# Kernel optimization log

Hardware: AMD Instinct MI355X
Metric: run time of the kernel (lower is better)

The kernel has to match this reference:

```python
import jax, jax.numpy as jnp
import numpy as np
import math

B, S, HID = 4, 512, 768
H, D = 12, 64          # heads, head_size
I = 3072               # intermediate_size
EPS = 1e-12


def setup_inputs() -> dict:
    key = jax.random.key(0)
    ks = jax.random.split(key, 16)
    std = 0.02
    inp = {
        'hidden_states': jax.random.normal(ks[0], (B, S, HID), jnp.float32),
        'attention_mask': jnp.zeros((B, 1, 1, S), jnp.float32),
        'Wq': jax.random.normal(ks[1], (HID, HID), jnp.float32) * std,
        'bq': jnp.zeros((HID,), jnp.float32),
        'Wk': jax.random.normal(ks[2], (HID, HID), jnp.float32) * std,
        'bk': jnp.zeros((HID,), jnp.float32),
        'Wv': jax.random.normal(ks[3], (HID, HID), jnp.float32) * std,
        'bv': jnp.zeros((HID,), jnp.float32),
        'Wo': jax.random.normal(ks[4], (H, D, HID), jnp.float32) * std,  # per-head w_o
        'bo': jnp.zeros((H, HID), jnp.float32),
        'w_kp': jax.nn.softmax(jax.random.normal(ks[5], (H,), jnp.float32)),
        'w_a': jax.nn.softmax(jax.random.normal(ks[6], (H,), jnp.float32)),
        'Wi': jax.random.normal(ks[7], (HID, I), jnp.float32) * std,
        'bi': jnp.zeros((I,), jnp.float32),
        'Wout': jax.random.normal(ks[8], (I, HID), jnp.float32) * std,
        'bout': jnp.zeros((HID,), jnp.float32),
        'gamma': jnp.ones((HID,), jnp.float32),
        'beta': jnp.zeros((HID,), jnp.float32),
    }
    return inp


def _layernorm(x, gamma, beta):
    u = x.mean(-1, keepdims=True)
    s = jnp.mean((x - u) ** 2, axis=-1, keepdims=True)
    return gamma * (x - u) / jnp.sqrt(s + EPS) + beta


def _gelu(x):
    return x * 0.5 * (1.0 + jax.lax.erf(x / math.sqrt(2.0)))


def reference(hidden_states, attention_mask, Wq, bq, Wk, bk, Wv, bv,
              Wo, bo, w_kp, w_a, Wi, bi, Wout, bout, gamma, beta):
    # self-attention (eval mode: no dropout, no head_mask)
    q = (hidden_states @ Wq + bq).reshape(B, S, H, D)
    k = (hidden_states @ Wk + bk).reshape(B, S, H, D)
    v = (hidden_states @ Wv + bv).reshape(B, S, H, D)
    scores = jnp.einsum('bqhd,bkhd->bhqk', q, k) / math.sqrt(D)
    scores = scores + attention_mask  # additive mask, broadcast [B,1,1,S]
    probs = jax.nn.softmax(scores, axis=-1)
    ctx = jnp.einsum('bhqk,bkhd->bqhd', probs, v)  # [B,S,H,D]

    # per-head output projection w_o[i]: 64 -> 768, scaled by kappa
    head_out = jnp.einsum('bqhd,hdm->bqhm', ctx, Wo) + bo  # [B,S,H,HID]
    x = w_kp[None, None, :, None] * head_out
    # shared intermediate (gelu) + output linear, applied per head stream
    inter = _gelu(jnp.einsum('bqhm,mi->bqhi', x, Wi) + bi)  # [B,S,H,I]
    out = jnp.einsum('bqhi,im->bqhm', inter, Wout) + bout   # [B,S,H,HID]
    out = (w_a[None, None, :, None] * out).sum(axis=2)      # sum over heads

    return _layernorm(hidden_states + out, gamma, beta)
```

## Files before the change

### kernel.cpp

```cpp
#include <hip/hip_runtime.h>
#include <hip/hip_bf16.h>
#include <math.h>

typedef __hip_bfloat16 bf16;
typedef __attribute__((ext_vector_type(4))) float f32x4;
typedef __attribute__((ext_vector_type(8))) short short8;
typedef __attribute__((ext_vector_type(4))) unsigned short u16x4;

#define HIDN 768
#define NTOK 2048
#define NH 12
#define HD 64
#define ISZ 3072
#define SEQ 512

__device__ __forceinline__ bf16 f2bf(float x){ return __float2bfloat16(x); }
__device__ __forceinline__ float bf2f(unsigned short u){ return __uint_as_float(((unsigned)u)<<16); }
__device__ __forceinline__ float gelu_fast(float x){
    float u = x*x;
    float g = fmaf(u, fmaf(u, 0.00340656f, -0.0530184f), 0.393242f);
    float phi = __builtin_amdgcn_fmed3f(fmaf(x, g, 0.5f), 0.f, 1.f);
    return x * phi;
}

__device__ __forceinline__ void gload16(const bf16* g, bf16* l){
    __builtin_amdgcn_global_load_lds(
        (const __attribute__((address_space(1))) unsigned int*)g,
        (__attribute__((address_space(3))) unsigned int*)l,
        16, 0, 0);
}

#define FENCE asm volatile("" ::: "memory")

template<int EPI>
__global__ __launch_bounds__(512)
void gemm_pipe(const bf16* __restrict__ A, const bf16* __restrict__ B,
               void* __restrict__ Cbase, const float* __restrict__ bias,
               int lda, int ldb, int ldc,
               long sAz, long sBz, long sCz)
{
    __shared__ __align__(16) char hlds[2*24576];
    int z = blockIdx.z;
    A += (long)z*sAz; B += (long)z*sBz;

    int nwg  = gridDim.x * gridDim.y;
    int orig = blockIdx.y * gridDim.x + blockIdx.x;
    int q8 = nwg >> 3, r8 = nwg & 7;
    int xcd = orig & 7, idx = orig >> 3;
    int wg = (xcd < r8 ? xcd*(q8+1) : r8*(q8+1) + (xcd-r8)*q8) + idx;
    int bn = wg % gridDim.x, bm = wg / gridDim.x;

    int t = threadIdx.x;
    int wave = t >> 6, lane = t & 63;
    int wm = (wave >> 1) << 5;
    int wn = (wave & 1) << 5;
    int lr = lane & 15, lg = lane >> 4;
    int x7 = lr & 7;
    int gb0 = ((lg    ) ^ x7) << 4;
    int gb1 = ((4 | lg) ^ x7) << 4;

    int srow = t >> 3;
    int glog = (t & 7) ^ (srow & 7);
    const bf16* Ag0 = A + (long)(bm*128 + srow)*lda + glog*8;
    const bf16* Ag1 = Ag0 + (long)64*lda;
    const bf16* Bg0 = B + (long)(bn*64 + srow)*ldb + glog*8;

#define PSTAGE(buf,kt) { \
    gload16(Ag0 + (kt)*64, (bf16*)(hlds + (buf)*24576 + t*16)); \
    gload16(Ag1 + (kt)*64, (bf16*)(hlds + (buf)*24576 + 8192 + t*16)); \
    gload16(Bg0 + (kt)*64, (bf16*)(hlds + (buf)*24576 + 16384 + t*16)); }

    PSTAGE(0, 0);

    f32x4 acc[2][2] = {};

    #pragma unroll
    for (int kt = 0; kt < 12; ++kt){
        if (kt < 11) PSTAGE((kt+1)&1, kt+1);
        if (kt < 11) asm volatile("s_waitcnt vmcnt(3)" ::: "memory");
        else         asm volatile("s_waitcnt vmcnt(0)" ::: "memory");
        FENCE; __builtin_amdgcn_s_barrier(); FENCE;

        const char* Lb = hlds + (kt&1)*24576;
        short8 af[2][2], bfr[2][2];
        #pragma unroll
        for (int m=0;m<2;m++){
            const char* pr = Lb + (wm + m*16 + lr)*128;
            af[m][0] = *(const short8*)(pr + gb0);
            af[m][1] = *(const short8*)(pr + gb1);
        }
        #pragma unroll
        for (int n=0;n<2;n++){
            const char* pr = Lb + 16384 + (wn + n*16 + lr)*128;
            bfr[n][0] = *(const short8*)(pr + gb0);
            bfr[n][1] = *(const short8*)(pr + gb1);
        }
        __builtin_amdgcn_s_setprio(1);
        #pragma unroll
        for (int m=0;m<2;m++)
            #pragma unroll
            for (int n=0;n<2;n++)
                #pragma unroll
                for (int kk=0;kk<2;kk++)
                    acc[m][n] = __builtin_amdgcn_mfma_f32_16x16x32_bf16(af[m][kk], bfr[n][kk], acc[m][n], 0,0,0);
        __builtin_amdgcn_s_setprio(0);
        FENCE; __builtin_amdgcn_s_barrier(); FENCE;
    }
#undef PSTAGE

    #pragma unroll
    for (int m=0;m<2;m++){
        #pragma unroll
        for (int n=0;n<2;n++){
            int col = bn*64 + wn + n*16 + lr;
            #pragma unroll
            for (int i=0;i<4;i++){
                long row = (long)bm*128 + wm + m*16 + lg*4 + i;
                ((bf16*)Cbase + (long)z*sCz)[row*ldc+col] = f2bf(acc[m][n][i]);
            }
        }
    }
}

__global__ __launch_bounds__(512)
void gemm_pre(const bf16* __restrict__ WiT, const bf16* __restrict__ Wobf,
              const bf16* __restrict__ bo_pad, const bf16* __restrict__ hbf,
              const bf16* __restrict__ WqkvT,
              bf16* __restrict__ WcT, float* __restrict__ bhc,
              bf16* __restrict__ qkv,
              const float* __restrict__ w_kp, const float* __restrict__ bi,
              const float* __restrict__ bqkv)
{
    __shared__ __align__(16) char hlds[2*24576];
    int bid = blockIdx.x;
    int mode, local, gx, nwg, ldc;
    const bf16 *A, *B;
    if (bid < 48){        mode=0; local=bid;     gx=48; nwg=48;  A=bo_pad; B=WiT;   ldc=ISZ; }
    else if (bid < 336){  mode=1; local=bid-48;  gx=12; nwg=288; A=WiT;    B=Wobf;  ldc=HIDN; }
    else {                mode=2; local=bid-336; gx=36; nwg=576; A=hbf;    B=WqkvT; ldc=3*HIDN; }

    int cpx = nwg >> 3;
    int wg = (local & 7)*cpx + (local >> 3);
    int bn = wg % gx, bm = wg / gx;

    int t = threadIdx.x;
    int wave = t >> 6, lane = t & 63;
    int wm = (wave >> 1) << 5;
    int wn = (wave & 1) << 5;
    int lr = lane & 15, lg = lane >> 4;
    int x7 = lr & 7;
    int gb0 = ((lg    ) ^ x7) << 4;
    int gb1 = ((4 | lg) ^ x7) << 4;

    int srow = t >> 3;
    int glog = (t & 7) ^ (srow & 7);
    const bf16* Ag0 = A + (long)(bm*128 + srow)*HIDN + glog*8;
    const bf16* Ag1 = Ag0 + (long)64*HIDN;
    const bf16* Bg0 = B + (long)(bn*64 + srow)*HIDN + glog*8;

#define PSTAGE(buf,kt) { \
    gload16(Ag0 + (kt)*64, (bf16*)(hlds + (buf)*24576 + t*16)); \
    gload16(Ag1 + (kt)*64, (bf16*)(hlds + (buf)*24576 + 8192 + t*16)); \
    gload16(Bg0 + (kt)*64, (bf16*)(hlds + (buf)*24576 + 16384 + t*16)); }

    PSTAGE(0, 0);

    f32x4 acc[2][2] = {};

    #pragma unroll
    for (int kt = 0; kt < 12; ++kt){
        if (kt < 11) PSTAGE((kt+1)&1, kt+1);
        if (kt < 11) asm volatile("s_waitcnt vmcnt(3)" ::: "memory");
        else         asm volatile("s_waitcnt vmcnt(0)" ::: "memory");
        FENCE; __builtin_amdgcn_s_barrier(); FENCE;

        const char* Lb = hlds + (kt&1)*24576;
        short8 af[2][2], bfr[2][2];
        #pragma unroll
        for (int m=0;m<2;m++){
            const char* pr = Lb + (wm + m*16 + lr)*128;
            af[m][0] = *(const short8*)(pr + gb0);
            af[m][1] = *(const short8*)(pr + gb1);
        }
        #pragma unroll
        for (int n=0;n<2;n++){
            const char* pr = Lb + 16384 + (wn + n*16 + lr)*128;
            bfr[n][0] = *(const short8*)(pr + gb0);
            bfr[n][1] = *(const short8*)(pr + gb1);
        }
        __builtin_amdgcn_s_setprio(1);
        #pragma unroll
        for (int m=0;m<2;m++)
            #pragma unroll
            for (int n=0;n<2;n++)
                #pragma unroll
                for (int kk=0;kk<2;kk++)
                    acc[m][n] = __builtin_amdgcn_mfma_f32_16x16x32_bf16(af[m][kk], bfr[n][kk], acc[m][n], 0,0,0);
        __builtin_amdgcn_s_setprio(0);
        FENCE; __builtin_amdgcn_s_barrier(); FENCE;
    }
#undef PSTAGE

    #pragma unroll
    for (int m=0;m<2;m++){
        #pragma unroll
        for (int n=0;n<2;n++){
            int col = bn*64 + wn + n*16 + lr;
            #pragma unroll
            for (int i=0;i<4;i++){
                long row = (long)bm*128 + wm + m*16 + lg*4 + i;
                float v = acc[m][n][i];
                if (mode == 0){
                    if (row < NH) bhc[row*ISZ+col] = fmaf(w_kp[row], v, bi[col]);
                } else if (mode == 1){
                    WcT[row*HIDN+col] = f2bf(v * w_kp[col>>6]);
                } else {
                    qkv[row*(3*HIDN)+col] = f2bf(v + bqkv[col]);
                }
            }
        }
    }
}

__global__ __launch_bounds__(256)
void flash_attn(const bf16* __restrict__ qkv, const bf16* __restrict__ Vt,
                const float* __restrict__ mask, bf16* __restrict__ ctx2)
{
    __shared__ __align__(16) char p_lds[4*2048];
    __shared__ float mrg[2][64][21];
    int z = blockIdx.y;
    int b = z / NH, h = z - b*NH;
    int t = threadIdx.x;
    int wave = t >> 6, lane = t & 63;
    int qg = wave >> 1, kh = wave & 1;
    int q0 = blockIdx.x*32 + qg*16;
    int lr = lane & 15, lg = lane >> 4;
    int x7 = lr & 7;
    int gb0 = ((lg    ) ^ x7) << 4;
    int gb1 = ((4 | lg) ^ x7) << 4;

    const bf16* Qp = qkv + (long)(b*SEQ + q0 + lr)*(3*HIDN) + h*HD + lg*8;
    short8 aq0 = *(const short8*)(Qp);
    short8 aq1 = *(const short8*)(Qp + 32);

    const bf16* Kb = qkv + (long)b*SEQ*(3*HIDN) + HIDN + h*HD + lg*8;
    const bf16* Vb = Vt + (long)z*HD*SEQ;
    const float* mb = mask + b*SEQ;
    char* pw = p_lds + wave*2048;

    f32x4 o[4] = {};
    float lsum[4] = {0.f,0.f,0.f,0.f};

    for (int kt = kh*4; kt < kh*4 + 4; ++kt){
        int kbase = kt*64;
        short8 bk0[4], bk1[4];
        #pragma unroll
        for (int nf=0;nf<4;nf++){
            const bf16* kp = Kb + (long)(kbase + nf*16 + lr)*(3*HIDN);
            bk0[nf] = *(const short8*)(kp);
            bk1[nf] = *(const short8*)(kp + 32);
        }
        f32x4 s[4] = {};
        #pragma unroll
        for (int nf=0;nf<4;nf++){
            s[nf] = __builtin_amdgcn_mfma_f32_16x16x32_bf16(aq0, bk0[nf], s[nf], 0,0,0);
            s[nf] = __builtin_amdgcn_mfma_f32_16x16x32_bf16(aq1, bk1[nf], s[nf], 0,0,0);
        }
        short8 bv0[4], bv1[4];
        #pragma unroll
        for (int nf=0;nf<4;nf++){
            const bf16* vp = Vb + (long)(nf*16 + lr)*SEQ + kbase + lg*8;
            bv0[nf] = *(const short8*)(vp);
            bv1[nf] = *(const short8*)(vp + 32);
        }
        #pragma unroll
        for (int nf=0;nf<4;nf++){
            float mk = mb[kbase + nf*16 + lr];
            int gk = nf*2 + (lr>>3);
            #pragma unroll
            for (int i=0;i<4;i++){
                int q = lg*4 + i;
                float e = __expf(fmaf(s[nf][i], 0.125f, mk));
                lsum[i] += e;
                *(bf16*)(pw + q*128 + ((gk ^ (q&7))<<4) + (lr&7)*2) = f2bf(e);
            }
        }
        short8 ap0 = *(const short8*)(pw + lr*128 + gb0);
        short8 ap1 = *(const short8*)(pw + lr*128 + gb1);
        #pragma unroll
        for (int nf=0;nf<4;nf++){
            o[nf] = __builtin_amdgcn_mfma_f32_16x16x32_bf16(ap0, bv0[nf], o[nf], 0,0,0);
            o[nf] = __builtin_amdgcn_mfma_f32_16x16x32_bf16(ap1, bv1[nf], o[nf], 0,0,0);
        }
    }

    if (kh == 1){
        float* m = &mrg[qg][lane][0];
        #pragma unroll
        for (int nf=0;nf<4;nf++)
            #pragma unroll
            for (int i=0;i<4;i++) m[nf*4+i] = o[nf][i];
        #pragma unroll
        for (int i=0;i<4;i++) m[16+i] = lsum[i];
    }
    __syncthreads();
    if (kh == 1) return;

    {
        const float* m = &mrg[qg][lane][0];
        #pragma unroll
        for (int nf=0;nf<4;nf++)
            #pragma unroll
            for (int i=0;i<4;i++) o[nf][i] += m[nf*4+i];
        #pragma unroll
        for (int i=0;i<4;i++) lsum[i] += m[16+i];
    }

    #pragma unroll
    for (int i=0;i<4;i++){
        float v = lsum[i];
        v += __shfl_xor(v, 1, 64);
        v += __shfl_xor(v, 2, 64);
        v += __shfl_xor(v, 4, 64);
        v += __shfl_xor(v, 8, 64);
        lsum[i] = __builtin_amdgcn_rcpf(v);
    }
    bf16* Cp = ctx2 + (long)(b*SEQ + q0)*HIDN + h*HD;
    #pragma unroll
    for (int nf=0;nf<4;nf++)
        #pragma unroll
        for (int i=0;i<4;i++)
            Cp[(long)(lg*4+i)*HIDN + nf*16 + lr] = f2bf(o[nf][i] * lsum[i]);
}

__global__ __launch_bounds__(512)
void gemm_heads(const bf16* __restrict__ A, const bf16* __restrict__ B,
                bf16* __restrict__ S, const float* __restrict__ bhc,
                const float* __restrict__ w_a)
{
    __shared__ __align__(16) char hlds[2*24576 + 3072];
    char* bhcl = hlds + 49152;

    int nwg  = gridDim.x * gridDim.y;
    int orig = blockIdx.y * gridDim.x + blockIdx.x;
    int cpx = nwg >> 3;
    int wg = (orig & 7)*cpx + (orig >> 3);
    int bn = wg % gridDim.x, bm = wg / gridDim.x;

    int t = threadIdx.x;
    int wave = t >> 6, lane = t & 63;
    int wm = (wave >> 1) << 5;
    int wn = (wave & 1) << 5;
    int lr = lane & 15, lg = lane >> 4;
    int x7 = lr & 7;
    int gb0 = ((lg    ) ^ x7) << 4;
    int gb1 = ((4 | lg) ^ x7) << 4;

    int srow = t >> 3;
    int glog = (t & 7) ^ (srow & 7);
    const bf16* Ag0 = A + (long)(bm*128 + srow)*HIDN + glog*8;
    const bf16* Ag1 = Ag0 + (long)64*HIDN;
    const bf16* Bg0 = B + (long)(bn*64 + srow)*HIDN + glog*8;

    float wav[NH];
    #pragma unroll
    for (int h=0;h<NH;h++) wav[h] = w_a[h];

    if (t < 192){
        const float* src = bhc + (t>>4)*ISZ + bn*64 + (t&15)*4;
        gload16((const bf16*)src, (bf16*)(bhcl + t*16));
    }

#define HSTAGE(buf,h) { \
    gload16(Ag0 + (h)*64, (bf16*)(hlds + (buf)*24576 + t*16)); \
    gload16(Ag1 + (h)*64, (bf16*)(hlds + (buf)*24576 + 8192 + t*16)); \
    gload16(Bg0 + (h)*64, (bf16*)(hlds + (buf)*24576 + 16384 + t*16)); }

    HSTAGE(0, 0);

    f32x4 acc[2][2] = {};
    f32x4 sacc[2][2] = {};

    #pragma unroll
    for (int h = 0; h < NH; ++h){
        if (h < NH-1) HSTAGE((h+1)&1, h+1);
        if (h > 0){
            float bh0 = *(const float*)(bhcl + (h-1)*256 + (wn+lr)*4);
            float bh1 = *(const float*)(bhcl + (h-1)*256 + (wn+16+lr)*4);
            #pragma unroll
            for (int m=0;m<2;m++)
                #pragma unroll
                for (int n=0;n<2;n++)
                    #pragma unroll
                    for (int i=0;i<4;i++){
                        float v = acc[m][n][i] + (n ? bh1 : bh0);
                        sacc[m][n][i] = fmaf(wav[h-1], gelu_fast(v), sacc[m][n][i]);
                        acc[m][n][i] = 0.f;
                    }
        }
        if (h < NH-1) asm volatile("s_waitcnt vmcnt(3)" ::: "memory");
        else          asm volatile("s_waitcnt vmcnt(0)" ::: "memory");
        FENCE; __builtin_amdgcn_s_barrier(); FENCE;

        const char* Lb = hlds + (h&1)*24576;
        short8 af[2][2], bfr[2][2];
        #pragma unroll
        for (int m=0;m<2;m++){
            const char* pr = Lb + (wm + m*16 + lr)*128;
            af[m][0] = *(const short8*)(pr + gb0);
            af[m][1] = *(const short8*)(pr + gb1);
        }
        #pragma unroll
        for (int n=0;n<2;n++){
            const char* pr = Lb + 16384 + (wn + n*16 + lr)*128;
            bfr[n][0] = *(const short8*)(pr + gb0);
            bfr[n][1] = *(const short8*)(pr + gb1);
        }
        __builtin_amdgcn_s_setprio(1);
        #pragma unroll
        for (int m=0;m<2;m++)
            #pragma unroll
            for (int n=0;n<2;n++)
                #pragma unroll
                for (int kk=0;kk<2;kk++)
                    acc[m][n] = __builtin_amdgcn_mfma_f32_16x16x32_bf16(af[m][kk], bfr[n][kk], acc[m][n], 0,0,0);
        __builtin_amdgcn_s_setprio(0);
        FENCE; __builtin_amdgcn_s_barrier(); FENCE;
    }
#undef HSTAGE

    {
        float bh0 = *(const float*)(bhcl + (NH-1)*256 + (wn+lr)*4);
        float bh1 = *(const float*)(bhcl + (NH-1)*256 + (wn+16+lr)*4);
        #pragma unroll
        for (int m=0;m<2;m++)
            #pragma unroll
            for (int n=0;n<2;n++)
                #pragma unroll
                for (int i=0;i<4;i++){
                    float v = acc[m][n][i] + (n ? bh1 : bh0);
                    sacc[m][n][i] = fmaf(wav[NH-1], gelu_fast(v), sacc[m][n][i]);
                }
    }

    #pragma unroll
    for (int m=0;m<2;m++)
        #pragma unroll
        for (int n=0;n<2;n++)
            #pragma unroll
            for (int i=0;i<4;i++){
                long row = (long)bm*128 + wm + m*16 + lg*4 + i;
                S[row*ISZ + bn*64 + wn + n*16 + lr] = f2bf(sacc[m][n][i]);
            }
}

#define NPREP (NTOK*HIDN + HIDN*HIDN + 128*HIDN + 3*HIDN)
__global__ __launch_bounds__(256)
void prep_all(const float* __restrict__ Wq, const float* __restrict__ Wk,
              const float* __restrict__ Wv, const float* __restrict__ Wi,
              const float* __restrict__ Wout,
              bf16* __restrict__ WqkvT, bf16* __restrict__ WiT,
              bf16* __restrict__ WoutT,
              const float* __restrict__ hidden, const float* __restrict__ Wo,
              const float* __restrict__ bq, const float* __restrict__ bk,
              const float* __restrict__ bv, const float* __restrict__ bo,
              bf16* __restrict__ hbf, bf16* __restrict__ Wobf,
              float* __restrict__ bqkv, bf16* __restrict__ bo_pad)
{
    __shared__ float tile[32][33];
    int bid = blockIdx.x;
    if (bid >= 6336){
        int i = (bid-6336)*256 + threadIdx.x;
        const int n1 = NTOK*HIDN, n2 = HIDN*HIDN, n3 = 128*HIDN;
        if (i < n1) hbf[i] = f2bf(hidden[i]);
        int j = i - n1;
        if (j >= 0 && j < n2) Wobf[j] = f2bf(Wo[j]);
        int k = i - n1 - n2;
        if (k >= 0 && k < n3) bo_pad[k] = (k < NH*HIDN) ? f2bf(bo[k]) : f2bf(0.f);
        int l = i - n1 - n2 - n3;
        if (l >= 0 && l < 3*HIDN)
            bqkv[l] = (l < HIDN) ? bq[l] : (l < 2*HIDN ? bk[l-HIDN] : bv[l-2*HIDN]);
        return;
    }
    const float* src; bf16* dst; int R, C, ct, rem;
    if (bid < 1728){
        int z = bid / 576; rem = bid - z*576;
        src = (z==0) ? Wq : ((z==1) ? Wk : Wv);
        dst = WqkvT + (long)z*HIDN*HIDN;
        R = HIDN; C = HIDN; ct = 24;
    } else if (bid < 4032){
        rem = bid - 1728; src = Wi; dst = WiT; R = HIDN; C = ISZ; ct = 96;
    } else {
        rem = bid - 4032; src = Wout; dst = WoutT; R = ISZ; C = HIDN; ct = 24;
    }
    int c0 = (rem % ct)*32, r0 = (rem / ct)*32;
    int tx = threadIdx.x & 31, ty = threadIdx.x >> 5;
    #pragma unroll
    for (int i=0;i<32;i+=8) tile[ty+i][tx] = src[(long)(r0+ty+i)*C + c0+tx];
    __syncthreads();
    #pragma unroll
    for (int i=0;i<32;i+=8) dst[(long)(c0+ty+i)*R + r0+tx] = f2bf(tile[tx][ty+i]);
}

__global__ __launch_bounds__(256)
void transpose_v(const bf16* __restrict__ qkv, bf16* __restrict__ Vt)
{
    __shared__ bf16 tile[32][33];
    int za = blockIdx.z; int b = za/NH, h = za - b*NH;
    const bf16* src = qkv + (long)b*SEQ*3*HIDN + 2*HIDN + h*HD;
    bf16* dst = Vt + (long)za*HD*SEQ;
    int d0 = blockIdx.x*32, s0 = blockIdx.y*32;
    int tx = threadIdx.x & 31, ty = threadIdx.x >> 5;
    #pragma unroll
    for (int i=0;i<32;i+=8) tile[ty+i][tx] = src[(long)(s0+ty+i)*(3*HIDN) + d0+tx];
    __syncthreads();
    #pragma unroll
    for (int i=0;i<32;i+=8) dst[(long)(d0+ty+i)*SEQ + s0+tx] = tile[tx][ty+i];
}

__global__ __launch_bounds__(192)
void add_ln(const float4* __restrict__ hidden, const u16x4* __restrict__ part,
            const float4* __restrict__ bout, const float* __restrict__ w_a,
            const float4* __restrict__ gamma, const float4* __restrict__ beta,
            float4* __restrict__ out)
{
    __shared__ float red[6];
    int row = blockIdx.x;
    int t = threadIdx.x;
    int wave = t >> 6, lane = t & 63;
    float swa = 0.f;
    #pragma unroll
    for (int h=0;h<NH;h++) swa += w_a[h];

    long idx = (long)row*192 + t;
    float4 x = hidden[idx];
    #pragma unroll
    for (int z=0;z<4;z++){
        u16x4 p = part[(long)z*NTOK*192 + idx];
        x.x += bf2f(p.x); x.y += bf2f(p.y); x.z += bf2f(p.z); x.w += bf2f(p.w);
    }
    float4 bo4 = bout[t];
    x.x += swa*bo4.x; x.y += swa*bo4.y; x.z += swa*bo4.z; x.w += swa*bo4.w;

    float sum = x.x + x.y + x.z + x.w;
    #pragma unroll
    for (int o=32;o>0;o>>=1) sum += __shfl_xor(sum,o,64);
    if (lane==0) red[wave] = sum;
    __syncthreads();
    sum = red[0] + red[1] + red[2];
    float u = sum * (1.0f/768.0f);

    float dx = x.x-u, dy = x.y-u, dz = x.z-u, dw = x.w-u;
    float vs = dx*dx + dy*dy + dz*dz + dw*dw;
    #pragma unroll
    for (int o=32;o>0;o>>=1) vs += __shfl_xor(vs,o,64);
    if (lane==0) red[3+wave] = vs;
    __syncthreads();
    vs = red[3] + red[4] + red[5];
    float rstd = rsqrtf(vs*(1.0f/768.0f) + 1e-12f);

    float4 g = gamma[t], b = beta[t];
    float4 r;
    r.x = g.x*dx*rstd + b.x;
    r.y = g.y*dy*rstd + b.y;
    r.z = g.z*dz*rstd + b.z;
    r.w = g.w*dw*rstd + b.w;
    out[idx] = r;
}

extern "C" void kernel_launch(void* const* d_in, const int* in_sizes, int n_in,
                              void* d_out, int out_size, void* d_ws, size_t ws_size,
                              hipStream_t stream)
{
    const float* hidden = (const float*)d_in[0];
    const float* mask   = (const float*)d_in[1];
    const float* Wq = (const float*)d_in[2];
    const float* bq = (const float*)d_in[3];
    const float* Wk = (const float*)d_in[4];
    const float* bk = (const float*)d_in[5];
    const float* Wv = (const float*)d_in[6];
    const float* bv = (const float*)d_in[7];
    const float* Wo = (const float*)d_in[8];
    const float* bo = (const float*)d_in[9];
    const float* w_kp = (const float*)d_in[10];
    const float* w_a  = (const float*)d_in[11];
    const float* Wi = (const float*)d_in[12];
    const float* bi = (const float*)d_in[13];
    const float* Wout = (const float*)d_in[14];
    const float* boutp = (const float*)d_in[15];
    const float* gamma = (const float*)d_in[16];
    const float* beta  = (const float*)d_in[17];
    float* out = (float*)d_out;

    char* w = (char*)d_ws;
    auto alloc = [&](size_t bytes)->char* {
        char* p = w; w += (bytes + 255) & ~(size_t)255; return p;
    };
    bf16*  hbf    = (bf16*) alloc((size_t)NTOK*HIDN*2);
    bf16*  WqkvT  = (bf16*) alloc((size_t)3*HIDN*HIDN*2);
    float* bqkv   = (float*)alloc((size_t)3*HIDN*4);
    bf16*  WiT    = (bf16*) alloc((size_t)ISZ*HIDN*2);
    bf16*  WoutT  = (bf16*) alloc((size_t)HIDN*ISZ*2);
    bf16*  Wobf   = (bf16*) alloc((size_t)HIDN*HIDN*2);
    bf16*  WcT    = (bf16*) alloc((size_t)ISZ*HIDN*2);
    bf16*  bo_pad = (bf16*) alloc((size_t)128*HIDN*2);
    float* bhc    = (float*)alloc((size_t)NH*ISZ*4);
    bf16*  part   = (bf16*) alloc((size_t)4*NTOK*HIDN*2);
    bf16*  qkv    = (bf16*) alloc((size_t)NTOK*3*HIDN*2);
    bf16*  ctx2   = (bf16*) alloc((size_t)NTOK*HIDN*2);
    bf16*  Sbuf   = (bf16*) alloc((size_t)NTOK*ISZ*2);
    bf16*  Vt     = (bf16*) alloc((size_t)NH*4*HD*SEQ*2);

    prep_all<<<6336 + (NPREP+255)/256, 256, 0, stream>>>(
        Wq, Wk, Wv, Wi, Wout, WqkvT, WiT, WoutT,
        hidden, Wo, bq, bk, bv, bo, hbf, Wobf, bqkv, bo_pad);

    gemm_pre<<<912, 512, 0, stream>>>(
        WiT, Wobf, bo_pad, hbf, WqkvT,
        WcT, bhc, qkv, w_kp, bi, bqkv);

    transpose_v<<<dim3(2,16,48), 256, 0, stream>>>(qkv, Vt);
    flash_attn<<<dim3(SEQ/32, 48), 256, 0, stream>>>(qkv, Vt, mask, ctx2);

    gemm_heads<<<dim3(ISZ/64, NTOK/128), 512, 0, stream>>>(
        ctx2, WcT, Sbuf, bhc, w_a);

    gemm_pipe<1><<<dim3(HIDN/64, NTOK/128, 4), 512, 0, stream>>>(
        Sbuf, WoutT, part, nullptr,
        ISZ, ISZ, HIDN,
        768, 768, (long)NTOK*HIDN);

    add_ln<<<NTOK, 192, 0, stream>>>(
        (const float4*)hidden, (const u16x4*)part, (const float4*)boutp,
        w_a, (const float4*)gamma, (const float4*)beta, (float4*)out);
}
```

Baseline: 110.5 us.

## Widen gemm_heads N tile from 64 to 96 columns per workgroup

Each workgroup of the per-head GEMM+GELU kernel now covers 96 output columns instead of 64, and each wave computes a 2x3 MFMA fragment grid instead of 2x2. This lets each A tile loaded from ctx2 be reused across more columns, cuts the grid from 768 to 512 workgroups, and lowers the A traffic per output. The bias table is now loaded synchronously into LDS, w_a is read per head instead of held in registers, and only six waves issue B loads, so the vmcnt waits become wave-dependent. The costs are more LDS and more accumulator registers per workgroup, with a possible loss of occupancy, and 512 workgroups may fill the CUs less evenly.

```diff
diff --git a/kernel.cpp b/kernel.cpp
--- a/kernel.cpp
+++ b/kernel.cpp
@@ -333,13 +333,13 @@
             Cp[(long)(lg*4+i)*HIDN + nf*16 + lr] = f2bf(o[nf][i] * lsum[i]);
 }
 
-__global__ __launch_bounds__(512)
+__global__ __launch_bounds__(512, 4)
 void gemm_heads(const bf16* __restrict__ A, const bf16* __restrict__ B,
                 bf16* __restrict__ S, const float* __restrict__ bhc,
                 const float* __restrict__ w_a)
 {
-    __shared__ __align__(16) char hlds[2*24576 + 3072];
-    char* bhcl = hlds + 49152;
+    __shared__ __align__(16) char hlds[2*28672 + 4608];
+    char* bhcl = hlds + 57344;
 
     int nwg  = gridDim.x * gridDim.y;
     int orig = blockIdx.y * gridDim.x + blockIdx.x;
@@ -350,7 +350,7 @@
     int t = threadIdx.x;
     int wave = t >> 6, lane = t & 63;
     int wm = (wave >> 1) << 5;
-    int wn = (wave & 1) << 5;
+    int wn = (wave & 1) * 48;
     int lr = lane & 15, lg = lane >> 4;
     int x7 = lr & 7;
     int gb0 = ((lg    ) ^ x7) << 4;
@@ -360,50 +360,59 @@
     int glog = (t & 7) ^ (srow & 7);
     const bf16* Ag0 = A + (long)(bm*128 + srow)*HIDN + glog*8;
     const bf16* Ag1 = Ag0 + (long)64*HIDN;
-    const bf16* Bg0 = B + (long)(bn*64 + srow)*HIDN + glog*8;
-
-    float wav[NH];
-    #pragma unroll
-    for (int h=0;h<NH;h++) wav[h] = w_a[h];
-
-    if (t < 192){
-        const float* src = bhc + (t>>4)*ISZ + bn*64 + (t&15)*4;
-        gload16((const bf16*)src, (bf16*)(bhcl + t*16));
-    }
+    const bf16* Bg0 = B + (long)(bn*96 + srow)*HIDN + glog*8;
+    const bf16* Bg1 = Bg0 + (long)48*HIDN;
+
+    if (t < 288){
+        int hh = t / 24, cc = (t % 24) * 4;
+        float4 v = *(const float4*)&bhc[hh*ISZ + bn*96 + cc];
+        *(float4*)(bhcl + t*16) = v;
+    }
+    asm volatile("s_waitcnt vmcnt(0)" ::: "memory");
 
 #define HSTAGE(buf,h) { \
-    gload16(Ag0 + (h)*64, (bf16*)(hlds + (buf)*24576 + t*16)); \
-    gload16(Ag1 + (h)*64, (bf16*)(hlds + (buf)*24576 + 8192 + t*16)); \
-    gload16(Bg0 + (h)*64, (bf16*)(hlds + (buf)*24576 + 16384 + t*16)); }
+    gload16(Ag0 + (h)*64, (bf16*)(hlds + (buf)*28672 + t*16)); \
+    gload16(Ag1 + (h)*64, (bf16*)(hlds + (buf)*28672 + 8192 + t*16)); \
+    if (wave < 6){ \
+        gload16(Bg0 + (h)*64, (bf16*)(hlds + (buf)*28672 + 16384 + t*16)); \
+        gload16(Bg1 + (h)*64, (bf16*)(hlds + (buf)*28672 + 22528 + t*16)); \
+    } }
 
     HSTAGE(0, 0);
 
-    f32x4 acc[2][2] = {};
-    f32x4 sacc[2][2] = {};
+    f32x4 acc[2][3] = {};
+    f32x4 sacc[2][3] = {};
 
     #pragma unroll
     for (int h = 0; h < NH; ++h){
         if (h < NH-1) HSTAGE((h+1)&1, h+1);
         if (h > 0){
-            float bh0 = *(const float*)(bhcl + (h-1)*256 + (wn+lr)*4);
-            float bh1 = *(const float*)(bhcl + (h-1)*256 + (wn+16+lr)*4);
+            float wa = w_a[h-1];
+            float bh[3];
+            #pragma unroll
+            for (int n=0;n<3;n++)
+                bh[n] = *(const float*)(bhcl + (h-1)*384 + (wn + n*16 + lr)*4);
             #pragma unroll
             for (int m=0;m<2;m++)
                 #pragma unroll
-                for (int n=0;n<2;n++)
+                for (int n=0;n<3;n++)
                     #pragma unroll
                     for (int i=0;i<4;i++){
-                        float v = acc[m][n][i] + (n ? bh1 : bh0);
-                        sacc[m][n][i] = fmaf(wav[h-1], gelu_fast(v), sacc[m][n][i]);
+                        float v = acc[m][n][i] + bh[n];
+                        sacc[m][n][i] = fmaf(wa, gelu_fast(v), sacc[m][n][i]);
                         acc[m][n][i] = 0.f;
                     }
         }
-        if (h < NH-1) asm volatile("s_waitcnt vmcnt(3)" ::: "memory");
-        else          asm volatile("s_waitcnt vmcnt(0)" ::: "memory");
+        if (h < NH-1){
+            if (wave < 6) asm volatile("s_waitcnt vmcnt(4)" ::: "memory");
+            else          asm volatile("s_waitcnt vmcnt(2)" ::: "memory");
+        } else {
+            asm volatile("s_waitcnt vmcnt(0)" ::: "memory");
+        }
         FENCE; __builtin_amdgcn_s_barrier(); FENCE;
 
-        const char* Lb = hlds + (h&1)*24576;
-        short8 af[2][2], bfr[2][2];
+        const char* Lb = hlds + (h&1)*28672;
+        short8 af[2][2], bfr[3][2];
         #pragma unroll
         for (int m=0;m<2;m++){
             const char* pr = Lb + (wm + m*16 + lr)*128;
@@ -411,7 +420,7 @@
             af[m][1] = *(const short8*)(pr + gb1);
         }
         #pragma unroll
-        for (int n=0;n<2;n++){
+        for (int n=0;n<3;n++){
             const char* pr = Lb + 16384 + (wn + n*16 + lr)*128;
             bfr[n][0] = *(const short8*)(pr + gb0);
             bfr[n][1] = *(const short8*)(pr + gb1);
@@ -420,7 +429,7 @@
         #pragma unroll
         for (int m=0;m<2;m++)
             #pragma unroll
-            for (int n=0;n<2;n++)
+            for (int n=0;n<3;n++)
                 #pragma unroll
                 for (int kk=0;kk<2;kk++)
                     acc[m][n] = __builtin_amdgcn_mfma_f32_16x16x32_bf16(af[m][kk], bfr[n][kk], acc[m][n], 0,0,0);
@@ -430,27 +439,30 @@
 #undef HSTAGE
 
     {
-        float bh0 = *(const float*)(bhcl + (NH-1)*256 + (wn+lr)*4);
-        float bh1 = *(const float*)(bhcl + (NH-1)*256 + (wn+16+lr)*4);
+        float wa = w_a[NH-1];
+        float bh[3];
+        #pragma unroll
+        for (int n=0;n<3;n++)
+            bh[n] = *(const float*)(bhcl + (NH-1)*384 + (wn + n*16 + lr)*4);
         #pragma unroll
         for (int m=0;m<2;m++)
             #pragma unroll
-            for (int n=0;n<2;n++)
+            for (int n=0;n<3;n++)
                 #pragma unroll
                 for (int i=0;i<4;i++){
-                    float v = acc[m][n][i] + (n ? bh1 : bh0);
-                    sacc[m][n][i] = fmaf(wav[NH-1], gelu_fast(v), sacc[m][n][i]);
+                    float v = acc[m][n][i] + bh[n];
+                    sacc[m][n][i] = fmaf(wa, gelu_fast(v), sacc[m][n][i]);
                 }
     }
 
     #pragma unroll
     for (int m=0;m<2;m++)
         #pragma unroll
-        for (int n=0;n<2;n++)
+        for (int n=0;n<3;n++)
             #pragma unroll
             for (int i=0;i<4;i++){
                 long row = (long)bm*128 + wm + m*16 + lg*4 + i;
-                S[row*ISZ + bn*64 + wn + n*16 + lr] = f2bf(sacc[m][n][i]);
+                S[row*ISZ + bn*96 + wn + n*16 + lr] = f2bf(sacc[m][n][i]);
             }
 }
 
@@ -622,7 +634,7 @@
     transpose_v<<<dim3(2,16,48), 256, 0, stream>>>(qkv, Vt);
     flash_attn<<<dim3(SEQ/32, 48), 256, 0, stream>>>(qkv, Vt, mask, ctx2);
 
-    gemm_heads<<<dim3(ISZ/64, NTOK/128), 512, 0, stream>>>(
+    gemm_heads<<<dim3(ISZ/96, NTOK/128), 512, 0, stream>>>(
         ctx2, WcT, Sbuf, bhc, w_a);
 
     gemm_pipe<1><<<dim3(HIDN/64, NTOK/128, 4), 512, 0, stream>>>(
```

After: 239.7 us. 2.17x slower.
